# Kernel tuning notes

Measured on AMD Instinct MI355X. Metric: run time of the kernel, lower is better.

## Reference

```python
import jax, jax.numpy as jnp
import numpy as np

B, C, V = 4096, 1000, 8000   # batch, NUM_COMPO, NUM_CHARS
THRESH = 0.8                 # compo_score_thresh
SCALE = 0.1                  # score_adjustment_scale
TOPK = 5


def setup_inputs() -> dict:
    key = jax.random.key(0)
    k1, k2, k3, k4 = jax.random.split(key, 4)
    return {
        "pred_class_logits": jax.random.normal(k1, (B, V), jnp.float32),
        "pred_compo_logits": jax.random.normal(k2, (B, C), jnp.float32),
        "compo_co_occurrence_prob": jax.random.uniform(k3, (C, C), dtype=jnp.float32),
        "compo_chinese_matrix": jax.random.randint(k4, (C, V), 0, 2, dtype=jnp.int32),
    }


def _decode_one(compo_scores, co_occ, matrix):
    """components_to_chinese_char for one sample. compo_scores:[C], co_occ:[C,C], matrix:[C,V]."""
    nC, nV = matrix.shape
    # score adjustment from co-occurrence of components above threshold
    sel = compo_scores > THRESH                                   # [C]
    adj = SCALE * jnp.sum(
        jnp.where(sel[:, None], co_occ * compo_scores[:, None], 0.0), axis=0)  # [C]
    scores = compo_scores + adj
    max_idx = jnp.argmax(scores)
    max_score = scores[max_idx]
    # re-threshold and sort selected scores descending (fixed-shape: mask with -inf)
    sel2 = scores > THRESH
    num_selected = jnp.sum(sel2.astype(jnp.int32))
    masked = jnp.where(sel2, scores, -jnp.inf)
    order = jnp.argsort(-masked)          # descending; selected compo indices first
    sorted_scores = masked[order]
    hit0 = matrix[max_idx]                # [V] 0/1

    def cond(carry):
        i, hit, _ = carry
        return (i < num_selected) & (jnp.sum(hit) > 1)

    def body(carry):
        i, hit, _ = carry
        row = matrix[order[i]]
        new_hit = jnp.where(hit + row == 2, 1, 0).astype(jnp.int32)  # intersection
        return (i + 1, new_hit, hit)

    i0 = jnp.array(1, jnp.int32)
    i, hit, prev = jax.lax.while_loop(cond, body, (i0, hit0, hit0))
    empty = jnp.sum(hit) == 0
    i = jnp.where(empty, i - 1, i)
    hit = jnp.where(empty, prev, hit)
    hit_score = jnp.where(i == 1, max_score, sorted_scores[jnp.maximum(i - 1, 0)])
    # first 5 hit char indices (ascending, as tf.where yields), padded with -1
    char_ids = jnp.where(hit == 1, jnp.arange(nV), nV)
    first5 = jnp.sort(char_ids)[:TOPK]
    hit_indices = jnp.where(first5 == nV, -1, first5).astype(jnp.int32)
    return hit_indices, hit_score


def reference(pred_class_logits, pred_compo_logits, compo_co_occurrence_prob, compo_chinese_matrix):
    class_probs = jax.nn.softmax(pred_class_logits, axis=1)            # [B,V]
    class_scores, class_indices = jax.lax.top_k(class_probs, TOPK)     # [B,5]
    compo_scores = jax.nn.sigmoid(pred_compo_logits)                   # [B,C]
    hit_indices, hit_scores = jax.vmap(_decode_one, in_axes=(0, None, None))(
        compo_scores, compo_co_occurrence_prob, compo_chinese_matrix)
    class_indices = class_indices.astype(jnp.int32)
    num_hit = jnp.sum((hit_indices != -1).astype(jnp.int32), axis=1)   # [B]
    combined1 = jnp.where(num_hit == 1, hit_indices[:, 0], class_indices[:, 0])
    combined2 = jnp.where((class_scores[:, 0] < 0.85) & (num_hit == 1),
                          hit_indices[:, 0], class_indices[:, 0])
    return (class_indices, class_scores, hit_indices, hit_scores, combined1, combined2)
```

## Files before the change

### kernel.cpp

```cpp
#include <hip/hip_runtime.h>
#include <cstdint>
#include <cstddef>

typedef unsigned long long u64;

#define B_SZ 4096
#define C_SZ 1000
#define V_SZ 8000
#define RW 128
#define THRESHF 0.8f
#define SCALEF 0.1f

#define OFF_CI 0
#define OFF_CS (B_SZ * 5)
#define OFF_HI (2 * B_SZ * 5)
#define OFF_HS (3 * B_SZ * 5)
#define OFF_C1 (3 * B_SZ * 5 + B_SZ)
#define OFF_C2 (3 * B_SZ * 5 + 2 * B_SZ)

__global__ __launch_bounds__(256) void pack_kernel(const int* __restrict__ mat,
                                                   u64* __restrict__ packed) {
  const int c = blockIdx.x;
  const int tid = threadIdx.x;
  const int lane = tid & 63;
  const int wv = tid >> 6;
  const int* row = mat + (size_t)c * V_SZ;
  for (int base = 0; base < 8192; base += 256) {
    const int k = base + tid;
    int v = 0;
    if (k < V_SZ) v = row[k];
    u64 msk = __ballot(v != 0);
    if (lane == 0) packed[(size_t)c * RW + ((base >> 6) + wv)] = msk;
  }
}

__global__ __launch_bounds__(256) void class_topk_kernel(const float* __restrict__ logits,
                                                         float* __restrict__ out) {
  const int b = blockIdx.x;
  const int tid = threadIdx.x;
  const int lane = tid & 63;
  const int wv = tid >> 6;
  const float* row = logits + (size_t)b * V_SZ;
  float v[32];
#pragma unroll
  for (int f = 0; f < 8; ++f) {
    const int base = (f << 10) + (tid << 2);
    if (base < V_SZ) {
      float4 x = *(const float4*)(row + base);
      v[4 * f + 0] = x.x; v[4 * f + 1] = x.y; v[4 * f + 2] = x.z; v[4 * f + 3] = x.w;
    } else {
      v[4 * f + 0] = -INFINITY; v[4 * f + 1] = -INFINITY;
      v[4 * f + 2] = -INFINITY; v[4 * f + 3] = -INFINITY;
    }
  }
  __shared__ float sred[4];
  __shared__ int sredi[4];
  float lm = -INFINITY;
#pragma unroll
  for (int q = 0; q < 32; ++q) lm = fmaxf(lm, v[q]);
#pragma unroll
  for (int o = 32; o >= 1; o >>= 1) lm = fmaxf(lm, __shfl_xor(lm, o));
  if (lane == 0) sred[wv] = lm;
  __syncthreads();
  const float m = fmaxf(fmaxf(sred[0], sred[1]), fmaxf(sred[2], sred[3]));
  float ls = 0.f;
#pragma unroll
  for (int q = 0; q < 32; ++q) ls += expf(v[q] - m);
#pragma unroll
  for (int o = 32; o >= 1; o >>= 1) ls += __shfl_xor(ls, o);
  __syncthreads();
  if (lane == 0) sred[wv] = ls;
  __syncthreads();
  const float ssum = sred[0] + sred[1] + sred[2] + sred[3];
  for (int r = 0; r < 5; ++r) {
    float bv = -INFINITY;
    int bi = 0;
#pragma unroll
    for (int q = 0; q < 32; ++q) {
      const int idx = ((q >> 2) << 10) + (tid << 2) + (q & 3);
      if (v[q] > bv) { bv = v[q]; bi = idx; }
    }
#pragma unroll
    for (int o = 32; o >= 1; o >>= 1) {
      float ov = __shfl_xor(bv, o);
      int oi = __shfl_xor(bi, o);
      if (ov > bv || (ov == bv && oi < bi)) { bv = ov; bi = oi; }
    }
    __syncthreads();
    if (lane == 0) { sred[wv] = bv; sredi[wv] = bi; }
    __syncthreads();
    bv = sred[0]; bi = sredi[0];
#pragma unroll
    for (int w = 1; w < 4; ++w) {
      if (sred[w] > bv || (sred[w] == bv && sredi[w] < bi)) { bv = sred[w]; bi = sredi[w]; }
    }
    if (((bi & 1023) >> 2) == tid) {
      const int sl = ((bi >> 10) << 2) | (bi & 3);
#pragma unroll
      for (int q = 0; q < 32; ++q)
        if (q == sl) v[q] = -INFINITY;
    }
    if (tid == 0) {
      out[OFF_CI + b * 5 + r] = (float)bi;
      out[OFF_CS + b * 5 + r] = expf(bv - m) / ssum;
    }
  }
}

__global__ __launch_bounds__(256, 8) void matvec_kernel(const float* __restrict__ compo_logits,
                                                        const float* __restrict__ co_occ,
                                                        float* __restrict__ fin_ws) {
  const int tid = threadIdx.x;
  const int lane = tid & 63;
  const int w = tid >> 6;
  const int bid = blockIdx.x;
  const int g = bid >> 3;
  const int r = bid & 7;
  const int h = r >> 2;
  const int sg = g * 4 + (r & 3);
  const int b = sg * 4 + w;
  __shared__ short s_idx[4][512];
  __shared__ float s_val[4][512];

  const float4* lg4 = (const float4*)(compo_logits + (size_t)b * C_SZ);
  float raw[16];
#pragma unroll
  for (int p = 0; p < 4; ++p) {
    const int fi = lane + (p << 6);
    if (fi < 250) {
      float4 x = lg4[fi];
      raw[4 * p + 0] = 1.0f / (1.0f + expf(-x.x));
      raw[4 * p + 1] = 1.0f / (1.0f + expf(-x.y));
      raw[4 * p + 2] = 1.0f / (1.0f + expf(-x.z));
      raw[4 * p + 3] = 1.0f / (1.0f + expf(-x.w));
    } else {
      raw[4 * p + 0] = 0.f; raw[4 * p + 1] = 0.f; raw[4 * p + 2] = 0.f; raw[4 * p + 3] = 0.f;
    }
  }
  int n = 0;
#pragma unroll
  for (int p = 0; p < 4; ++p) {
    unsigned mb = 0;
    if (raw[4 * p + 0] > THRESHF) mb |= 1u;
    if (raw[4 * p + 1] > THRESHF) mb |= 2u;
    if (raw[4 * p + 2] > THRESHF) mb |= 4u;
    if (raw[4 * p + 3] > THRESHF) mb |= 8u;
    const int cnt = __popc(mb);
    int inc = cnt;
#pragma unroll
    for (int o = 1; o < 64; o <<= 1) {
      int t = __shfl_up(inc, o);
      if (lane >= o) inc += t;
    }
    int off = n + inc - cnt;
    const int total = __shfl(inc, 63);
#pragma unroll
    for (int j = 0; j < 4; ++j) {
      if (mb & (1u << j)) {
        s_idx[w][off] = (short)((p << 8) + (lane << 2) + j);
        s_val[w][off] = raw[4 * p + j];
        ++off;
      }
    }
    n += total;
  }
  if (lane < 2) { s_idx[w][n + lane] = 0; s_val[w][n + lane] = 0.0f; }

  float4 accA = {0, 0, 0, 0}, accB = {0, 0, 0, 0};
  {
    const float4* cop = (const float4*)co_occ;
    const int f4a = (h << 7) + lane;
    const int f4b = f4a + 64;
    const bool gb = (h == 0) || (lane < 58);
    for (int e = 0; e < n; e += 2) {
      const int i0 = s_idx[w][e + 0]; const float m0 = s_val[w][e + 0];
      const int i1 = s_idx[w][e + 1]; const float m1 = s_val[w][e + 1];
      const float4* r0 = cop + (size_t)i0 * 250;
      const float4* r1 = cop + (size_t)i1 * 250;
      const float4 a0 = r0[f4a];
      const float4 a1 = r1[f4a];
      float4 b0 = {0, 0, 0, 0}, b1 = {0, 0, 0, 0};
      if (gb) { b0 = r0[f4b]; b1 = r1[f4b]; }
      accA.x += m0 * a0.x; accA.y += m0 * a0.y; accA.z += m0 * a0.z; accA.w += m0 * a0.w;
      accB.x += m0 * b0.x; accB.y += m0 * b0.y; accB.z += m0 * b0.z; accB.w += m0 * b0.w;
      accA.x += m1 * a1.x; accA.y += m1 * a1.y; accA.z += m1 * a1.z; accA.w += m1 * a1.w;
      accB.x += m1 * b1.x; accB.y += m1 * b1.y; accB.z += m1 * b1.z; accB.w += m1 * b1.w;
    }
  }
  float* dst = fin_ws + (size_t)b * C_SZ;
  float4 oA, oB;
  if (h == 0) {
    oA.x = raw[0] + SCALEF * accA.x; oA.y = raw[1] + SCALEF * accA.y;
    oA.z = raw[2] + SCALEF * accA.z; oA.w = raw[3] + SCALEF * accA.w;
    oB.x = raw[4] + SCALEF * accB.x; oB.y = raw[5] + SCALEF * accB.y;
    oB.z = raw[6] + SCALEF * accB.z; oB.w = raw[7] + SCALEF * accB.w;
    *(float4*)(dst + (lane << 2)) = oA;
    *(float4*)(dst + 256 + (lane << 2)) = oB;
  } else {
    oA.x = raw[8] + SCALEF * accA.x;  oA.y = raw[9] + SCALEF * accA.y;
    oA.z = raw[10] + SCALEF * accA.z; oA.w = raw[11] + SCALEF * accA.w;
    oB.x = raw[12] + SCALEF * accB.x; oB.y = raw[13] + SCALEF * accB.y;
    oB.z = raw[14] + SCALEF * accB.z; oB.w = raw[15] + SCALEF * accB.w;
    *(float4*)(dst + 512 + (lane << 2)) = oA;
    if (lane < 58) *(float4*)(dst + 768 + (lane << 2)) = oB;
  }
}

__global__ __launch_bounds__(256, 4) void tail_kernel(const float* __restrict__ sc_arr,
                                                      const u64* __restrict__ packed,
                                                      float* __restrict__ out) {
  const int b = blockIdx.x * 4 + (threadIdx.x >> 6);
  const int lane = threadIdx.x & 63;
  const float* sc = sc_arr + (size_t)b * C_SZ;
  u64 key[16];
  unsigned avail = 0;
  int cnt = 0;
  u64 kb = 0;
#pragma unroll
  for (int q = 0; q < 16; ++q) {
    const int col = lane + (q << 6);
    if (col < C_SZ) {
      const float s = sc[col];
      const u64 k = ((u64)__float_as_uint(s) << 32) | (u64)(0xFFFFFFFFu - (unsigned)col);
      key[q] = k;
      if (k > kb) kb = k;
      if (s > THRESHF) { avail |= 1u << q; cnt++; }
    } else key[q] = 0;
  }
  u64 mk = kb;
#pragma unroll
  for (int o = 32; o >= 1; o >>= 1) { u64 t = __shfl_xor(mk, o); if (t > mk) mk = t; }
  const float mxv = __uint_as_float((unsigned)(mk >> 32));
  const int mxi = (int)(0xFFFFFFFFu - (unsigned)(mk & 0xFFFFFFFFull));
#pragma unroll
  for (int o = 32; o >= 1; o >>= 1) cnt += __shfl_xor(cnt, o);
  const int nsel = cnt;
  if ((mxi & 63) == lane) avail &= ~(1u << (mxi >> 6));
  const u64* pr = packed + (size_t)mxi * RW;
  u64 h0 = pr[lane], h1 = pr[64 + lane];
  int pc = __popcll(h0) + __popcll(h1);
#pragma unroll
  for (int o = 32; o >= 1; o >>= 1) pc += __shfl_xor(pc, o);
  int i = 1;
  float last_val = mxv;
  if (nsel >= 2 && pc > 1) {
    for (;;) {
      int kt = (nsel - i < 8) ? (nsel - i) : 8;
      float cval[8];
      int cidx[8];
      u64 rl[8], rh[8];
      float lastc = last_val;
      int kv = 0;
#pragma unroll
      for (int k = 0; k < 8; ++k) {
        cval[k] = 0.0f; cidx[k] = -1;
        if (k < kt) {
          u64 lm = 0;
#pragma unroll
          for (int q = 0; q < 16; ++q)
            if (avail & (1u << q)) { if (key[q] > lm) lm = key[q]; }
          u64 ck = lm;
#pragma unroll
          for (int o = 32; o >= 1; o >>= 1) { u64 t = __shfl_xor(ck, o); if (t > ck) ck = t; }
          if (ck != 0) {
            cval[k] = __uint_as_float((unsigned)(ck >> 32));
            cidx[k] = (int)(0xFFFFFFFFu - (unsigned)(ck & 0xFFFFFFFFull));
            if ((cidx[k] & 63) == lane) avail &= ~(1u << (cidx[k] >> 6));
            lastc = cval[k];
            kv = k + 1;
          }
        }
      }
      kt = kv;
      if (kt == 0) break;
#pragma unroll
      for (int k = 0; k < 8; ++k) {
        if (k < kt) {
          const u64* rp = packed + (size_t)cidx[k] * RW;
          rl[k] = rp[lane]; rh[k] = rp[64 + lane];
        } else { rl[k] = ~0ull; rh[k] = ~0ull; }
      }
      u64 c0 = h0, c1 = h1, pk0 = 0, pk1 = 0;
#pragma unroll
      for (int k = 0; k < 8; ++k) {
        c0 &= rl[k]; c1 &= rh[k];
        const u64 p = (u64)(__popcll(c0) + __popcll(c1));
        if (k < 4) pk0 |= p << (k * 16); else pk1 |= p << ((k - 4) * 16);
      }
#pragma unroll
      for (int o = 32; o >= 1; o >>= 1) { pk0 += __shfl_xor(pk0, o); pk1 += __shfl_xor(pk1, o); }
      int kstar = -1;
      unsigned pcv = 0;
#pragma unroll
      for (int k = 0; k < 8; ++k) {
        if (k < kt && kstar < 0) {
          const unsigned f = (unsigned)(((k < 4 ? pk0 : pk1) >> ((k & 3) * 16)) & 0xFFFFull);
          if (f <= 1u) { kstar = k; pcv = f; }
        }
      }
      if (kstar >= 0) {
        float vk = 0.f, vkm1 = last_val;
#pragma unroll
        for (int k = 0; k < 8; ++k)
          if (k == kstar) { vk = cval[k]; if (k > 0) vkm1 = cval[k - 1]; }
        const int na = (pcv == 1u) ? (kstar + 1) : kstar;
#pragma unroll
        for (int k = 0; k < 8; ++k) if (k < na) { h0 &= rl[k]; h1 &= rh[k]; }
        if (pcv == 1u) { i += kstar + 1; last_val = vk; }
        else { i += kstar; last_val = vkm1; }
        break;
      }
#pragma unroll
      for (int k = 0; k < 8; ++k) if (k < kt) { h0 &= rl[k]; h1 &= rh[k]; }
      i += kt;
      last_val = lastc;
      if (i >= nsel) break;
    }
  }
  const float hit_score = (i == 1) ? mxv : last_val;

  const int c0n = __popcll(h0), c1n = __popcll(h1);
  int s0 = c0n;
#pragma unroll
  for (int o = 1; o < 64; o <<= 1) {
    int n = __shfl_up(s0, o);
    if (lane >= o) s0 += n;
  }
  const int tot0 = __shfl(s0, 63);
  const int pre0 = s0 - c0n;
  int s1 = c1n;
#pragma unroll
  for (int o = 1; o < 64; o <<= 1) {
    int n = __shfl_up(s1, o);
    if (lane >= o) s1 += n;
  }
  const int tot = tot0 + __shfl(s1, 63);
  const int pre1 = tot0 + s1 - c1n;
  {
    u64 x = h0;
    int r = pre0;
    while (x && r < 5) {
      const int bp = __ffsll((unsigned long long)x) - 1;
      out[OFF_HI + b * 5 + r] = (float)((lane << 6) + bp);
      x &= x - 1;
      ++r;
    }
    x = h1;
    r = pre1;
    while (x && r < 5) {
      const int bp = __ffsll((unsigned long long)x) - 1;
      out[OFF_HI + b * 5 + r] = (float)(((64 + lane) << 6) + bp);
      x &= x - 1;
      ++r;
    }
  }
  int fb = 0x7fffffff;
  if (c0n) fb = (lane << 6) + __ffsll((unsigned long long)h0) - 1;
  else if (c1n) fb = ((64 + lane) << 6) + __ffsll((unsigned long long)h1) - 1;
#pragma unroll
  for (int o = 32; o >= 1; o >>= 1) fb = min(fb, __shfl_xor(fb, o));
  if (lane == 0) {
    const int num_hit = tot < 5 ? tot : 5;
    for (int r = num_hit; r < 5; ++r) out[OFF_HI + b * 5 + r] = -1.0f;
    out[OFF_HS + b] = hit_score;
    const float ci0 = out[OFF_CI + b * 5];
    const float cs0 = out[OFF_CS + b * 5];
    out[OFF_C1 + b] = (num_hit == 1) ? (float)fb : ci0;
    out[OFF_C2 + b] = (cs0 < 0.85f && num_hit == 1) ? (float)fb : ci0;
  }
}

extern "C" void kernel_launch(void* const* d_in, const int* in_sizes, int n_in,
                              void* d_out, int out_size, void* d_ws, size_t ws_size,
                              hipStream_t stream) {
  (void)in_sizes; (void)n_in; (void)out_size; (void)ws_size;
  const float* class_logits = (const float*)d_in[0];
  const float* compo_logits = (const float*)d_in[1];
  const float* co_occ = (const float*)d_in[2];
  const int* mat = (const int*)d_in[3];
  float* out = (float*)d_out;
  u64* packed = (u64*)d_ws;
  float* fin_ws = (float*)((char*)d_ws + (size_t)C_SZ * RW * 8);

  pack_kernel<<<C_SZ, 256, 0, stream>>>(mat, packed);
  class_topk_kernel<<<B_SZ, 256, 0, stream>>>(class_logits, out);
  matvec_kernel<<<B_SZ / 2, 256, 0, stream>>>(compo_logits, co_occ, fin_ws);
  tail_kernel<<<B_SZ / 4, 256, 0, stream>>>(fin_ws, packed, out);
}
```

Before: 148.6 us.

## Fuse score-adjustment matvec and tail decode into one kernel via shared memory

Merges the co-occurrence matvec kernel and the tail decode kernel into a single decode_kernel. The adjusted scores stay in shared memory instead of making a round trip through a global workspace. Each block handles two samples, with two waves splitting the columns for the matvec, and only the first wave runs the decode. The co-occurrence loop is unrolled to four rows per iteration to expose more loads. The cost is that half the waves sit idle during the serial decode phase, and the extra shared memory and registers lower the occupancy target from 8 to 6.

After: 174.4 us. +17.4%, slower.

```diff
diff --git a/kernel.cpp b/kernel.cpp
--- a/kernel.cpp
+++ b/kernel.cpp
@@ -107,28 +107,28 @@
   }
 }
 
-__global__ __launch_bounds__(256, 8) void matvec_kernel(const float* __restrict__ compo_logits,
+__global__ __launch_bounds__(256, 6) void decode_kernel(const float* __restrict__ compo_logits,
                                                         const float* __restrict__ co_occ,
-                                                        float* __restrict__ fin_ws) {
+                                                        const u64* __restrict__ packed,
+                                                        float* __restrict__ out) {
   const int tid = threadIdx.x;
   const int lane = tid & 63;
   const int w = tid >> 6;
-  const int bid = blockIdx.x;
-  const int g = bid >> 3;
-  const int r = bid & 7;
-  const int h = r >> 2;
-  const int sg = g * 4 + (r & 3);
-  const int b = sg * 4 + w;
-  __shared__ short s_idx[4][512];
-  __shared__ float s_val[4][512];
-
-  const float4* lg4 = (const float4*)(compo_logits + (size_t)b * C_SZ);
+  const int sp = w >> 1;
+  const int h = w & 1;
+  const int b = blockIdx.x * 2 + sp;
+  __shared__ short s_idx[2][512];
+  __shared__ float s_val[2][512];
+  __shared__ float s_fin[2][1024];
+  __shared__ int s_n[2];
+
+  const float* lg = compo_logits + (size_t)b * C_SZ;
   float raw[16];
 #pragma unroll
   for (int p = 0; p < 4; ++p) {
     const int fi = lane + (p << 6);
     if (fi < 250) {
-      float4 x = lg4[fi];
+      float4 x = *(const float4*)(lg + (fi << 2));
       raw[4 * p + 0] = 1.0f / (1.0f + expf(-x.x));
       raw[4 * p + 1] = 1.0f / (1.0f + expf(-x.y));
       raw[4 * p + 2] = 1.0f / (1.0f + expf(-x.z));
@@ -137,34 +137,39 @@
       raw[4 * p + 0] = 0.f; raw[4 * p + 1] = 0.f; raw[4 * p + 2] = 0.f; raw[4 * p + 3] = 0.f;
     }
   }
-  int n = 0;
-#pragma unroll
-  for (int p = 0; p < 4; ++p) {
-    unsigned mb = 0;
-    if (raw[4 * p + 0] > THRESHF) mb |= 1u;
-    if (raw[4 * p + 1] > THRESHF) mb |= 2u;
-    if (raw[4 * p + 2] > THRESHF) mb |= 4u;
-    if (raw[4 * p + 3] > THRESHF) mb |= 8u;
-    const int cnt = __popc(mb);
-    int inc = cnt;
-#pragma unroll
-    for (int o = 1; o < 64; o <<= 1) {
-      int t = __shfl_up(inc, o);
-      if (lane >= o) inc += t;
-    }
-    int off = n + inc - cnt;
-    const int total = __shfl(inc, 63);
-#pragma unroll
-    for (int j = 0; j < 4; ++j) {
-      if (mb & (1u << j)) {
-        s_idx[w][off] = (short)((p << 8) + (lane << 2) + j);
-        s_val[w][off] = raw[4 * p + j];
-        ++off;
-      }
-    }
-    n += total;
-  }
-  if (lane < 2) { s_idx[w][n + lane] = 0; s_val[w][n + lane] = 0.0f; }
+  if (h == 0) {
+    int n = 0;
+#pragma unroll
+    for (int p = 0; p < 4; ++p) {
+      unsigned mb = 0;
+      if (raw[4 * p + 0] > THRESHF) mb |= 1u;
+      if (raw[4 * p + 1] > THRESHF) mb |= 2u;
+      if (raw[4 * p + 2] > THRESHF) mb |= 4u;
+      if (raw[4 * p + 3] > THRESHF) mb |= 8u;
+      const int cnt = __popc(mb);
+      int inc = cnt;
+#pragma unroll
+      for (int o = 1; o < 64; o <<= 1) {
+        int t = __shfl_up(inc, o);
+        if (lane >= o) inc += t;
+      }
+      int off = n + inc - cnt;
+      const int total = __shfl(inc, 63);
+#pragma unroll
+      for (int j = 0; j < 4; ++j) {
+        if (mb & (1u << j)) {
+          s_idx[sp][off] = (short)((p << 8) + (lane << 2) + j);
+          s_val[sp][off] = raw[4 * p + j];
+          ++off;
+        }
+      }
+      n += total;
+    }
+    if (lane < 4) { s_idx[sp][n + lane] = 0; s_val[sp][n + lane] = 0.0f; }
+    if (lane == 0) s_n[sp] = n;
+  }
+  __syncthreads();
+  const int n = s_n[sp];
 
   float4 accA = {0, 0, 0, 0}, accB = {0, 0, 0, 0};
   {
@@ -172,46 +177,48 @@
     const int f4a = (h << 7) + lane;
     const int f4b = f4a + 64;
     const bool gb = (h == 0) || (lane < 58);
-    for (int e = 0; e < n; e += 2) {
-      const int i0 = s_idx[w][e + 0]; const float m0 = s_val[w][e + 0];
-      const int i1 = s_idx[w][e + 1]; const float m1 = s_val[w][e + 1];
+    for (int e = 0; e < n; e += 4) {
+      const int i0 = s_idx[sp][e + 0]; const float m0 = s_val[sp][e + 0];
+      const int i1 = s_idx[sp][e + 1]; const float m1 = s_val[sp][e + 1];
+      const int i2 = s_idx[sp][e + 2]; const float m2 = s_val[sp][e + 2];
+      const int i3 = s_idx[sp][e + 3]; const float m3 = s_val[sp][e + 3];
       const float4* r0 = cop + (size_t)i0 * 250;
       const float4* r1 = cop + (size_t)i1 * 250;
-      const float4 a0 = r0[f4a];
-      const float4 a1 = r1[f4a];
-      float4 b0 = {0, 0, 0, 0}, b1 = {0, 0, 0, 0};
-      if (gb) { b0 = r0[f4b]; b1 = r1[f4b]; }
+      const float4* r2 = cop + (size_t)i2 * 250;
+      const float4* r3 = cop + (size_t)i3 * 250;
+      float4 a0 = r0[f4a], b0 = r1[f4a], d0 = r2[f4a], e0 = r3[f4a];
+      float4 a1 = {0, 0, 0, 0}, b1 = {0, 0, 0, 0}, d1 = {0, 0, 0, 0}, e1 = {0, 0, 0, 0};
+      if (gb) { a1 = r0[f4b]; b1 = r1[f4b]; d1 = r2[f4b]; e1 = r3[f4b]; }
       accA.x += m0 * a0.x; accA.y += m0 * a0.y; accA.z += m0 * a0.z; accA.w += m0 * a0.w;
-      accB.x += m0 * b0.x; accB.y += m0 * b0.y; accB.z += m0 * b0.z; accB.w += m0 * b0.w;
-      accA.x += m1 * a1.x; accA.y += m1 * a1.y; accA.z += m1 * a1.z; accA.w += m1 * a1.w;
+      accB.x += m0 * a1.x; accB.y += m0 * a1.y; accB.z += m0 * a1.z; accB.w += m0 * a1.w;
+      accA.x += m1 * b0.x; accA.y += m1 * b0.y; accA.z += m1 * b0.z; accA.w += m1 * b0.w;
       accB.x += m1 * b1.x; accB.y += m1 * b1.y; accB.z += m1 * b1.z; accB.w += m1 * b1.w;
-    }
-  }
-  float* dst = fin_ws + (size_t)b * C_SZ;
-  float4 oA, oB;
+      accA.x += m2 * d0.x; accA.y += m2 * d0.y; accA.z += m2 * d0.z; accA.w += m2 * d0.w;
+      accB.x += m2 * d1.x; accB.y += m2 * d1.y; accB.z += m2 * d1.z; accB.w += m2 * d1.w;
+      accA.x += m3 * e0.x; accA.y += m3 * e0.y; accA.z += m3 * e0.z; accA.w += m3 * e0.w;
+      accB.x += m3 * e1.x; accB.y += m3 * e1.y; accB.z += m3 * e1.z; accB.w += m3 * e1.w;
+    }
+  }
   if (h == 0) {
+    float4 oA, oB;
     oA.x = raw[0] + SCALEF * accA.x; oA.y = raw[1] + SCALEF * accA.y;
     oA.z = raw[2] + SCALEF * accA.z; oA.w = raw[3] + SCALEF * accA.w;
     oB.x = raw[4] + SCALEF * accB.x; oB.y = raw[5] + SCALEF * accB.y;
     oB.z = raw[6] + SCALEF * accB.z; oB.w = raw[7] + SCALEF * accB.w;
-    *(float4*)(dst + (lane << 2)) = oA;
-    *(float4*)(dst + 256 + (lane << 2)) = oB;
+    *(float4*)&s_fin[sp][(lane << 2)] = oA;
+    *(float4*)&s_fin[sp][256 + (lane << 2)] = oB;
   } else {
+    float4 oA, oB;
     oA.x = raw[8] + SCALEF * accA.x;  oA.y = raw[9] + SCALEF * accA.y;
     oA.z = raw[10] + SCALEF * accA.z; oA.w = raw[11] + SCALEF * accA.w;
     oB.x = raw[12] + SCALEF * accB.x; oB.y = raw[13] + SCALEF * accB.y;
     oB.z = raw[14] + SCALEF * accB.z; oB.w = raw[15] + SCALEF * accB.w;
-    *(float4*)(dst + 512 + (lane << 2)) = oA;
-    if (lane < 58) *(float4*)(dst + 768 + (lane << 2)) = oB;
-  }
-}
-
-__global__ __launch_bounds__(256, 4) void tail_kernel(const float* __restrict__ sc_arr,
-                                                      const u64* __restrict__ packed,
-                                                      float* __restrict__ out) {
-  const int b = blockIdx.x * 4 + (threadIdx.x >> 6);
-  const int lane = threadIdx.x & 63;
-  const float* sc = sc_arr + (size_t)b * C_SZ;
+    *(float4*)&s_fin[sp][512 + (lane << 2)] = oA;
+    if (lane < 58) *(float4*)&s_fin[sp][768 + (lane << 2)] = oB;
+  }
+  __syncthreads();
+  if (h == 1) return;
+
   u64 key[16];
   unsigned avail = 0;
   int cnt = 0;
@@ -220,7 +227,7 @@
   for (int q = 0; q < 16; ++q) {
     const int col = lane + (q << 6);
     if (col < C_SZ) {
-      const float s = sc[col];
+      const float s = s_fin[sp][col];
       const u64 k = ((u64)__float_as_uint(s) << 32) | (u64)(0xFFFFFFFFu - (unsigned)col);
       key[q] = k;
       if (k > kb) kb = k;
@@ -323,16 +330,16 @@
   int s0 = c0n;
 #pragma unroll
   for (int o = 1; o < 64; o <<= 1) {
-    int n = __shfl_up(s0, o);
-    if (lane >= o) s0 += n;
+    int nn = __shfl_up(s0, o);
+    if (lane >= o) s0 += nn;
   }
   const int tot0 = __shfl(s0, 63);
   const int pre0 = s0 - c0n;
   int s1 = c1n;
 #pragma unroll
   for (int o = 1; o < 64; o <<= 1) {
-    int n = __shfl_up(s1, o);
-    if (lane >= o) s1 += n;
+    int nn = __shfl_up(s1, o);
+    if (lane >= o) s1 += nn;
   }
   const int tot = tot0 + __shfl(s1, 63);
   const int pre1 = tot0 + s1 - c1n;
@@ -380,10 +387,8 @@
   const int* mat = (const int*)d_in[3];
   float* out = (float*)d_out;
   u64* packed = (u64*)d_ws;
-  float* fin_ws = (float*)((char*)d_ws + (size_t)C_SZ * RW * 8);
 
   pack_kernel<<<C_SZ, 256, 0, stream>>>(mat, packed);
   class_topk_kernel<<<B_SZ, 256, 0, stream>>>(class_logits, out);
-  matvec_kernel<<<B_SZ / 2, 256, 0, stream>>>(compo_logits, co_occ, fin_ws);
-  tail_kernel<<<B_SZ / 4, 256, 0, stream>>>(fin_ws, packed, out);
+  decode_kernel<<<B_SZ / 2, 256, 0, stream>>>(compo_logits, co_occ, packed, out);
 }
```
